# Performance work log

Measured on AMD Instinct MI355X. Metric: run time of the kernel, lower is better.

Reference implementation:

```python
import jax, jax.numpy as jnp
import numpy as np
import math

MODEL_DIM = 1024
B, S = 4, 2048


def setup_inputs() -> dict:
    key = jax.random.key(0)
    k_x, k_q, k_k, k_v = jax.random.split(key, 4)
    r5 = math.sqrt(5)
    x = jax.random.normal(k_x, (B, S, MODEL_DIM), dtype=jnp.float32)
    Q = jax.random.uniform(k_q, (MODEL_DIM, MODEL_DIM), minval=-r5, maxval=r5, dtype=jnp.float32)
    K = jax.random.uniform(k_k, (MODEL_DIM, MODEL_DIM), minval=-r5, maxval=r5, dtype=jnp.float32)
    V = jax.random.uniform(k_v, (MODEL_DIM, MODEL_DIM), minval=-r5, maxval=r5, dtype=jnp.float32)
    # attention_input == 'both' -> a == model_dim -> F is the full identity
    F = jnp.eye(MODEL_DIM, dtype=jnp.float32)
    return {"x": x, "Q": Q, "K": K, "V": V, "F": F}


def reference(x, Q, K, V, F):
    d = x.shape[-1]
    xf = jnp.matmul(x, F)
    Qx = jnp.matmul(xf, Q)          # [B,S,D]
    Kx = jnp.matmul(xf, K)          # [B,S,D]
    Vx = jnp.matmul(x, V)           # [B,S,D]
    scores = jnp.einsum('bqd,bkd->bqk', Qx, Kx) / math.sqrt(d)  # [B,S,S]
    seq = x.shape[1]
    mask = jnp.triu(jnp.ones((seq, seq), dtype=bool), k=1)
    scores = jnp.where(mask, -jnp.inf, scores)
    probs = jax.nn.softmax(scores, axis=-1)
    out = jnp.matmul(probs, Vx)     # [B,S,D]
    return (out, probs)
```

## Files before the change

kernel.cpp:

```cpp
#include <hip/hip_runtime.h>
#include <hip/hip_fp16.h>

typedef _Float16 f16;
typedef __attribute__((ext_vector_type(8))) _Float16 f16x8;
typedef __attribute__((ext_vector_type(4))) _Float16 f16x4;
typedef __attribute__((ext_vector_type(4))) float    f32x4;

#define D_MODEL 1024
#define SEQ     2048
#define BATCH   4
#define M_TOT   (BATCH * SEQ)
#define NE      ((long)M_TOT * D_MODEL)
#define WE      ((long)D_MODEL * D_MODEL)
#define OUT_ELEMS  ((long)M_TOT * D_MODEL)

static __device__ __forceinline__ f16x8 frag_read(const f16* lds, int row, int c)
{
    const f16x8* L = (const f16x8*)lds;
    return L[row * 4 + (c ^ ((row >> 1) & 3))];
}

static __device__ __forceinline__ void stage_tile(const f16* __restrict__ g, int row0,
                                                  int ld, int k0, f16* ldsbase,
                                                  int wave, int lane)
{
#pragma unroll
    for (int j = 0; j < 2; ++j) {
        const int chunk = wave * 2 + j;
        const int off16 = chunk * 64 + lane;
        const int row   = off16 >> 2;
        const int slot  = (off16 & 3) ^ ((row >> 1) & 3);
        const f16* src = g + (long)(row0 + row) * ld + (k0 + slot * 8);
        f16* dst = ldsbase + chunk * 512;
        __builtin_amdgcn_global_load_lds((const __attribute__((address_space(1))) void*)src,
                                         (__attribute__((address_space(3))) void*)dst,
                                         16, 0, 0);
    }
}

template<int ROWS>
static __device__ __forceinline__ void stage8(const f16* __restrict__ g, int row0,
                                              int ld, int k0, f16* dstbase,
                                              int wave, int lane)
{
#pragma unroll
    for (int j = 0; j < ROWS / 128; ++j) {
        const int off16 = j * 512 + wave * 64 + lane;
        const int row   = off16 >> 2;
        const int slot  = (off16 & 3) ^ ((row >> 1) & 3);
        const f16* src = g + (long)(row0 + row) * ld + (k0 + slot * 8);
        f16* dst = dstbase + (j * 512 + wave * 64) * 8;
        __builtin_amdgcn_global_load_lds((const __attribute__((address_space(1))) void*)src,
                                         (__attribute__((address_space(3))) void*)dst,
                                         16, 0, 0);
    }
}

#define BUFE 24576

template<int DUAL>
static __device__ __forceinline__ void g8_issueA(const f16* Ah, const f16* Al, int ld,
                                                 int m0, f16* lds, int t, int wave, int lane)
{
    f16* b = lds + (t & 1) * BUFE;
    stage8<256>(Ah, m0, ld, t * 32, b, wave, lane);
    if constexpr (DUAL) stage8<256>(Al, m0, ld, t * 32, b + 8192, wave, lane);
}
static __device__ __forceinline__ void g8_issueBh(const f16* BTh, int ld, int n0,
                                                  f16* lds, int t, int wave, int lane)
{
    stage8<128>(BTh, n0, ld, t * 32, lds + (t & 1) * BUFE + 16384, wave, lane);
}
static __device__ __forceinline__ void g8_issueBl(const f16* BTl, int ld, int n0,
                                                  f16* lds, int t, int wave, int lane)
{
    stage8<128>(BTl, n0, ld, t * 32, lds + (t & 1) * BUFE + 20480, wave, lane);
}

template<int DUAL>
static __device__ __forceinline__ void gemm8_pipe(
    const f16* __restrict__ Ah, const f16* __restrict__ Al,
    const f16* __restrict__ BTh, const f16* __restrict__ BTl,
    int ld, int m0, int n0, f16* lds, f32x4 acc[4][4], int wave, int lane)
{
    const int wr = wave >> 1, wc = wave & 1;
    const int cf = lane >> 4;

#pragma unroll
    for (int mi = 0; mi < 4; ++mi)
#pragma unroll
        for (int ni = 0; ni < 4; ++ni) acc[mi][ni] = (f32x4){0.f, 0.f, 0.f, 0.f};

    g8_issueA<DUAL>(Ah, Al, ld, m0, lds, 0, wave, lane);
    g8_issueBh(BTh, ld, n0, lds, 0, wave, lane);
    if constexpr (DUAL) g8_issueBl(BTl, ld, n0, lds, 0, wave, lane);
    g8_issueA<DUAL>(Ah, Al, ld, m0, lds, 1, wave, lane);
    g8_issueBh(BTh, ld, n0, lds, 1, wave, lane);

    for (int t = 0; t < 32; ++t) {
        if (t < 31) {
            if constexpr (DUAL) {
                g8_issueBl(BTl, ld, n0, lds, t + 1, wave, lane);
                asm volatile("s_waitcnt vmcnt(6)" ::: "memory");
            } else {
                asm volatile("s_waitcnt vmcnt(3)" ::: "memory");
            }
        } else {
            asm volatile("s_waitcnt vmcnt(0)" ::: "memory");
        }
        __builtin_amdgcn_sched_barrier(0);
        __builtin_amdgcn_s_barrier();
        __builtin_amdgcn_sched_barrier(0);

        f16* buf = lds + (t & 1) * BUFE;
        f16x8 fah[4], fal[4], fbh[4], fbl[4];
#pragma unroll
        for (int i = 0; i < 4; ++i) {
            const int ra = wr * 64 + i * 16 + (lane & 15);
            fah[i] = frag_read(buf, ra, cf);
            if constexpr (DUAL) fal[i] = frag_read(buf + 8192, ra, cf);
            const int rb = wc * 64 + i * 16 + (lane & 15);
            fbh[i] = frag_read(buf + 16384, rb, cf);
            if constexpr (DUAL) fbl[i] = frag_read(buf + 20480, rb, cf);
        }
        asm volatile("s_waitcnt lgkmcnt(0)" ::: "memory");
        __builtin_amdgcn_sched_barrier(0);
        __builtin_amdgcn_s_barrier();
        __builtin_amdgcn_sched_barrier(0);

        if (t < 30) {
            g8_issueA<DUAL>(Ah, Al, ld, m0, lds, t + 2, wave, lane);
            g8_issueBh(BTh, ld, n0, lds, t + 2, wave, lane);
        }
        __builtin_amdgcn_sched_barrier(0);

        __builtin_amdgcn_s_setprio(1);
#pragma unroll
        for (int mi = 0; mi < 4; ++mi)
#pragma unroll
            for (int ni = 0; ni < 4; ++ni)
                acc[mi][ni] = __builtin_amdgcn_mfma_f32_16x16x32_f16(fah[mi], fbh[ni], acc[mi][ni], 0, 0, 0);
        if constexpr (DUAL) {
#pragma unroll
            for (int mi = 0; mi < 4; ++mi)
#pragma unroll
                for (int ni = 0; ni < 4; ++ni)
                    acc[mi][ni] = __builtin_amdgcn_mfma_f32_16x16x32_f16(fah[mi], fbl[ni], acc[mi][ni], 0, 0, 0);
#pragma unroll
            for (int mi = 0; mi < 4; ++mi)
#pragma unroll
                for (int ni = 0; ni < 4; ++ni)
                    acc[mi][ni] = __builtin_amdgcn_mfma_f32_16x16x32_f16(fal[mi], fbh[ni], acc[mi][ni], 0, 0, 0);
        }
        __builtin_amdgcn_s_setprio(0);
    }
}

__global__ __launch_bounds__(512, 2) void k_gemm_T(
    const f16* __restrict__ xh, const f16* __restrict__ xl,
    const f16* __restrict__ WhT, const f16* __restrict__ WlT,
    f16* __restrict__ Th, f16* __restrict__ Tl)
{
    __shared__ __align__(16) f16 lds[49152];
    const int lane = threadIdx.x & 63, wave = threadIdx.x >> 6;
    const int L = blockIdx.x;
    const int swz = (L & 7) * 32 + (L >> 3);
    const int m0 = (swz >> 3) * 256;
    const int n0 = (swz & 7) * 128;
    f32x4 acc[4][4];
    gemm8_pipe<1>(xh, xl, WhT, WlT, D_MODEL, m0, n0, lds, acc, wave, lane);
    const int wr = wave >> 1, wc = wave & 1;
#pragma unroll
    for (int mi = 0; mi < 4; ++mi)
#pragma unroll
        for (int ni = 0; ni < 4; ++ni) {
            const int gn = n0 + wc * 64 + ni * 16 + (lane & 15);
#pragma unroll
            for (int r = 0; r < 4; ++r) {
                const int gm = m0 + wr * 64 + mi * 16 + (lane >> 4) * 4 + r;
                const float v = acc[mi][ni][r];
                const f16 h = (f16)v;
                Th[(long)gm * D_MODEL + gn] = h;
                Tl[(long)gm * D_MODEL + gn] = (f16)(v - (float)h);
            }
        }
}

__global__ __launch_bounds__(512, 2) void k_mega1(
    const f16* __restrict__ Th, const f16* __restrict__ Tl,
    const f16* __restrict__ xh, const f16* __restrict__ xl,
    const f16* __restrict__ VhT,
    float* __restrict__ scores, f16* __restrict__ VxT)
{
    __shared__ __align__(16) f16 lds[49152];
    const int lane = threadIdx.x & 63, wave = threadIdx.x >> 6;
    const int wr = wave >> 1, wc = wave & 1;
    f32x4 acc[4][4];

    if (blockIdx.x < 288) {
        const int L = blockIdx.x;
        const int swz = (L & 7) * 36 + (L >> 3);
        const int b = swz / 72;
        const int t = swz - b * 72;
        int qt = (int)((sqrtf(4.f * (float)t + 1.f) - 1.f) * 0.5f);
        while ((qt + 1) * (qt + 2) <= t) ++qt;
        while (qt * (qt + 1) > t) --qt;
        const int kt = t - qt * (qt + 1);

        const long ob = (long)b * SEQ * D_MODEL;
        gemm8_pipe<1>(Th + ob, Tl + ob, xh + ob, xl + ob, D_MODEL,
                      qt * 256, kt * 128, lds, acc, wave, lane);

        float* sb = scores + (long)b * SEQ * SEQ;
#pragma unroll
        for (int mi = 0; mi < 4; ++mi)
#pragma unroll
            for (int ni = 0; ni < 4; ++ni) {
                const int k = kt * 128 + wc * 64 + ni * 16 + (lane & 15);
#pragma unroll
                for (int r = 0; r < 4; ++r) {
                    const int q = qt * 256 + wr * 64 + mi * 16 + (lane >> 4) * 4 + r;
                    sb[(long)q * SEQ + k] = acc[mi][ni][r] * 0.03125f;
                }
            }
    } else {
        const int idx = blockIdx.x - 288;
        const int m0 = (idx >> 3) * 256;
        const int n0 = (idx & 7) * 128;
        gemm8_pipe<0>(xh, nullptr, VhT, nullptr, D_MODEL, m0, n0, lds, acc, wave, lane);
#pragma unroll
        for (int mi = 0; mi < 4; ++mi) {
            const int gm0 = m0 + wr * 64 + mi * 16 + (lane >> 4) * 4;
            const int b = gm0 >> 11, s = gm0 & 2047;
#pragma unroll
            for (int ni = 0; ni < 4; ++ni) {
                const int gn = n0 + wc * 64 + ni * 16 + (lane & 15);
                f16x4 p = {(f16)acc[mi][ni][0], (f16)acc[mi][ni][1],
                           (f16)acc[mi][ni][2], (f16)acc[mi][ni][3]};
                *(f16x4*)(VxT + ((long)b * D_MODEL + gn) * SEQ + s) = p;
            }
        }
    }
}

template<int DUAL>
static __device__ __forceinline__ void gemm_core(
    const f16* __restrict__ Ah, const f16* __restrict__ Al,
    const f16* __restrict__ BTh, const f16* __restrict__ BTl,
    int ld, int m0, int n0, int kEnd, f16* lds, f32x4 acc[4][4])
{
    const int t = threadIdx.x;
    const int lane = t & 63;
    const int wave = t >> 6;
    const int wr = wave >> 1, wc = wave & 1;
    const int cfrag = lane >> 4;

#pragma unroll
    for (int mi = 0; mi < 4; ++mi)
#pragma unroll
        for (int ni = 0; ni < 4; ++ni)
            acc[mi][ni] = (f32x4){0.f, 0.f, 0.f, 0.f};

    for (int k0 = 0; k0 < kEnd; k0 += 32) {
        stage_tile(Ah,  m0, ld, k0, lds,         wave, lane);
        stage_tile(BTh, n0, ld, k0, lds + 4096,  wave, lane);
        if (DUAL) {
            stage_tile(Al,  m0, ld, k0, lds + 8192,  wave, lane);
            stage_tile(BTl, n0, ld, k0, lds + 12288, wave, lane);
        }
        __syncthreads();

        f16x8 fah[4], fbh[4];
#pragma unroll
        for (int i = 0; i < 4; ++i) {
            fah[i] = frag_read(lds,        wr * 64 + i * 16 + (lane & 15), cfrag);
            fbh[i] = frag_read(lds + 4096, wc * 64 + i * 16 + (lane & 15), cfrag);
        }
        if (DUAL) {
            f16x8 fal[4], fbl[4];
#pragma unroll
            for (int i = 0; i < 4; ++i) {
                fal[i] = frag_read(lds + 8192,  wr * 64 + i * 16 + (lane & 15), cfrag);
                fbl[i] = frag_read(lds + 12288, wc * 64 + i * 16 + (lane & 15), cfrag);
            }
#pragma unroll
            for (int mi = 0; mi < 4; ++mi)
#pragma unroll
                for (int ni = 0; ni < 4; ++ni) {
                    acc[mi][ni] = __builtin_amdgcn_mfma_f32_16x16x32_f16(fah[mi], fbh[ni], acc[mi][ni], 0, 0, 0);
                    acc[mi][ni] = __builtin_amdgcn_mfma_f32_16x16x32_f16(fah[mi], fbl[ni], acc[mi][ni], 0, 0, 0);
                    acc[mi][ni] = __builtin_amdgcn_mfma_f32_16x16x32_f16(fal[mi], fbh[ni], acc[mi][ni], 0, 0, 0);
                }
        } else {
#pragma unroll
            for (int mi = 0; mi < 4; ++mi)
#pragma unroll
                for (int ni = 0; ni < 4; ++ni)
                    acc[mi][ni] = __builtin_amdgcn_mfma_f32_16x16x32_f16(fah[mi], fbh[ni], acc[mi][ni], 0, 0, 0);
        }
        __syncthreads();
    }
}

__global__ __launch_bounds__(256) void k_split_all(
    const float* __restrict__ x, const float* __restrict__ Q,
    const float* __restrict__ K, const float* __restrict__ V,
    f16* __restrict__ xh, f16* __restrict__ xl,
    f16* __restrict__ Qh, f16* __restrict__ Ql,
    f16* __restrict__ Kh, f16* __restrict__ Kl,
    f16* __restrict__ VhT)
{
    __shared__ float tile[32][33];
    const int bid = blockIdx.x;
    if (bid < 10240) {
        const float* src; f16 *dh, *dl; long off;
        if (bid < 8192)      { src = x; dh = xh; dl = xl; off = (long)bid * 1024; }
        else if (bid < 9216) { src = Q; dh = Qh; dl = Ql; off = (long)(bid - 8192) * 1024; }
        else                 { src = K; dh = Kh; dl = Kl; off = (long)(bid - 9216) * 1024; }
        const long i = off + threadIdx.x * 4;
        float4 v = *(const float4*)(src + i);
        f16 h0 = (f16)v.x, h1 = (f16)v.y, h2 = (f16)v.z, h3 = (f16)v.w;
        f16x4 hh = {h0, h1, h2, h3};
        f16x4 ll = {(f16)(v.x - (float)h0), (f16)(v.y - (float)h1),
                    (f16)(v.z - (float)h2), (f16)(v.w - (float)h3)};
        *(f16x4*)(dh + i) = hh;
        *(f16x4*)(dl + i) = ll;
    } else {
        const int idx = bid - 10240;
        const int n0 = (idx & 31) * 32, k0 = (idx >> 5) * 32;
        const int c = threadIdx.x & 31, r8 = threadIdx.x >> 5;
#pragma unroll
        for (int i = 0; i < 4; ++i) {
            const int r = r8 + i * 8;
            tile[r][c] = V[(long)(k0 + r) * D_MODEL + n0 + c];
        }
        __syncthreads();
#pragma unroll
        for (int i = 0; i < 4; ++i) {
            const int r = r8 + i * 8;
            VhT[(long)(n0 + r) * D_MODEL + k0 + c] = (f16)tile[c][r];
        }
    }
}

__global__ __launch_bounds__(256, 2) void k_gemm_w(
    const f16* __restrict__ Qh, const f16* __restrict__ Ql,
    const f16* __restrict__ Kh, const f16* __restrict__ Kl,
    f16* __restrict__ WhT, f16* __restrict__ WlT)
{
    __shared__ __align__(16) f16 lds[16384];
    f32x4 acc[4][4];
    const int m0 = blockIdx.y * 128, n0 = blockIdx.x * 128;
    gemm_core<1>(Qh, Ql, Kh, Kl, D_MODEL, m0, n0, D_MODEL, lds, acc);
    const int lane = threadIdx.x & 63, wave = threadIdx.x >> 6;
    const int wr = wave >> 1, wc = wave & 1;
#pragma unroll
    for (int mi = 0; mi < 4; ++mi)
#pragma unroll
        for (int ni = 0; ni < 4; ++ni) {
            const int gn = n0 + wc * 64 + ni * 16 + (lane & 15);
#pragma unroll
            for (int r = 0; r < 4; ++r) {
                const int gm = m0 + wr * 64 + mi * 16 + (lane >> 4) * 4 + r;
                const float v = acc[mi][ni][r];
                const f16 h = (f16)v;
                WhT[(long)gn * D_MODEL + gm] = h;
                WlT[(long)gn * D_MODEL + gm] = (f16)(v - (float)h);
            }
        }
}

__global__ __launch_bounds__(256) void k_softmax(float* __restrict__ probs,
                                                 f16* __restrict__ probs16)
{
    const long row = blockIdx.x;
    const int q = (int)(row & (SEQ - 1));
    float* s = probs + row * SEQ;
    const int t = threadIdx.x;
    const int kb = t * 8;
    float4 u0 = *(const float4*)(s + kb);
    float4 u1 = *(const float4*)(s + kb + 4);
    float v[8] = {u0.x, u0.y, u0.z, u0.w, u1.x, u1.y, u1.z, u1.w};
    float mx = -3.0e38f;
#pragma unroll
    for (int j = 0; j < 8; ++j) if (kb + j <= q) mx = fmaxf(mx, v[j]);
#pragma unroll
    for (int off = 32; off > 0; off >>= 1) mx = fmaxf(mx, __shfl_xor(mx, off, 64));
    __shared__ float redA[4], redB[4];
    const int lane = t & 63, wave = t >> 6;
    if (lane == 0) redA[wave] = mx;
    __syncthreads();
    mx = fmaxf(fmaxf(redA[0], redA[1]), fmaxf(redA[2], redA[3]));
    float e[8]; float sum = 0.f;
#pragma unroll
    for (int j = 0; j < 8; ++j) { e[j] = (kb + j <= q) ? __expf(v[j] - mx) : 0.f; sum += e[j]; }
#pragma unroll
    for (int off = 32; off > 0; off >>= 1) sum += __shfl_xor(sum, off, 64);
    if (lane == 0) redB[wave] = sum;
    __syncthreads();
    sum = (redB[0] + redB[1]) + (redB[2] + redB[3]);
    const float inv = 1.f / sum;
    float4 w0 = {e[0] * inv, e[1] * inv, e[2] * inv, e[3] * inv};
    float4 w1 = {e[4] * inv, e[5] * inv, e[6] * inv, e[7] * inv};
    *(float4*)(s + kb) = w0;
    *(float4*)(s + kb + 4) = w1;
    f16x8 p16 = {(f16)w0.x, (f16)w0.y, (f16)w0.z, (f16)w0.w,
                 (f16)w1.x, (f16)w1.y, (f16)w1.z, (f16)w1.w};
    *(f16x8*)(probs16 + row * SEQ + kb) = p16;
}

__global__ __launch_bounds__(256, 2) void k_gemm_pv(
    const f16* __restrict__ P, const f16* __restrict__ VT, float* __restrict__ out)
{
    const int dt = blockIdx.x, qt = 15 - blockIdx.y, b = blockIdx.z;
    __shared__ __align__(16) f16 lds[8192];
    f32x4 acc[4][4];
    const f16* Pb  = P  + (long)b * SEQ * SEQ;
    const f16* VTb = VT + (long)b * D_MODEL * SEQ;
    gemm_core<0>(Pb, nullptr, VTb, nullptr, SEQ, qt * 128, dt * 128, (qt + 1) * 128, lds, acc);
    float* ob = out + (long)b * SEQ * D_MODEL;
    const int lane = threadIdx.x & 63, wave = threadIdx.x >> 6;
    const int wr = wave >> 1, wc = wave & 1;
#pragma unroll
    for (int mi = 0; mi < 4; ++mi)
#pragma unroll
        for (int ni = 0; ni < 4; ++ni) {
            const int d = dt * 128 + wc * 64 + ni * 16 + (lane & 15);
#pragma unroll
            for (int r = 0; r < 4; ++r) {
                const int qq = qt * 128 + wr * 64 + mi * 16 + (lane >> 4) * 4 + r;
                ob[(long)qq * D_MODEL + d] = acc[mi][ni][r];
            }
        }
}

extern "C" void kernel_launch(void* const* d_in, const int* in_sizes, int n_in,
                              void* d_out, int out_size, void* d_ws, size_t ws_size,
                              hipStream_t stream)
{
    const float* x = (const float*)d_in[0];
    const float* Q = (const float*)d_in[1];
    const float* K = (const float*)d_in[2];
    const float* V = (const float*)d_in[3];

    float* out   = (float*)d_out;
    float* probs = out + OUT_ELEMS;

    f16* base = (f16*)d_ws;
    f16* xh   = base;
    f16* xl   = base + NE;
    f16* Th   = base + 2 * NE;
    f16* Tl   = base + 3 * NE;
    f16* VxT  = base + 4 * NE;
    f16* Qh   = base + 5 * NE;
    f16* Ql   = Qh + WE;
    f16* Kh   = Qh + 2 * WE;
    f16* Kl   = Qh + 3 * WE;
    f16* WhT  = Qh + 4 * WE;
    f16* WlT  = Qh + 5 * WE;
    f16* VhT  = Qh + 6 * WE;
    f16* probs16 = base + 2 * NE;

    k_split_all<<<11264, 256, 0, stream>>>(x, Q, K, V, xh, xl, Qh, Ql, Kh, Kl, VhT);
    k_gemm_w<<<dim3(8, 8), 256, 0, stream>>>(Qh, Ql, Kh, Kl, WhT, WlT);
    k_gemm_T<<<256, 512, 0, stream>>>(xh, xl, WhT, WlT, Th, Tl);
    k_mega1<<<544, 512, 0, stream>>>(Th, Tl, xh, xl, VhT, probs, VxT);
    k_softmax<<<8192, 256, 0, stream>>>(probs, probs16);
    k_gemm_pv<<<dim3(8, 16, 4), 256, 0, stream>>>(probs16, VxT, out);
}
```

Before: 274.3 us.

## Serialize dual-precision GEMM passes, shrink LDS, and move PV to pipelined 256x128 kernel

The dual-precision GEMM no longer loads hi and lo tiles together. It now runs three sequential K passes (hi*hi, hi*lo, lo*hi) through one half-size double-buffered pipeline. This cuts LDS per block so occupancy bounds rise from 2 to 4 blocks per CU. The PV product moves onto the same async global_load_lds pipeline with 256x128 tiles. The change also interleaves score and V blocks in the mega kernel, uses nontemporal stores for scores and probabilities, makes the split kernel handle 4 vectors per thread, and skips loading masked score entries in softmax. The risks are more pipeline iterations with fewer MFMAs each, and heavier register pressure at the higher occupancy target.

Measured after the change: 295.7 us. 7.8% more time.

```diff
diff --git a/kernel.cpp b/kernel.cpp
--- a/kernel.cpp
+++ b/kernel.cpp
@@ -56,32 +56,30 @@
     }
 }
 
-#define BUFE 24576
-
-template<int DUAL>
-static __device__ __forceinline__ void g8_issueA(const f16* Ah, const f16* Al, int ld,
-                                                 int m0, f16* lds, int t, int wave, int lane)
-{
-    f16* b = lds + (t & 1) * BUFE;
-    stage8<256>(Ah, m0, ld, t * 32, b, wave, lane);
-    if constexpr (DUAL) stage8<256>(Al, m0, ld, t * 32, b + 8192, wave, lane);
-}
-static __device__ __forceinline__ void g8_issueBh(const f16* BTh, int ld, int n0,
-                                                  f16* lds, int t, int wave, int lane)
-{
-    stage8<128>(BTh, n0, ld, t * 32, lds + (t & 1) * BUFE + 16384, wave, lane);
-}
-static __device__ __forceinline__ void g8_issueBl(const f16* BTl, int ld, int n0,
-                                                  f16* lds, int t, int wave, int lane)
-{
-    stage8<128>(BTl, n0, ld, t * 32, lds + (t & 1) * BUFE + 20480, wave, lane);
-}
-
-template<int DUAL>
-static __device__ __forceinline__ void gemm8_pipe(
-    const f16* __restrict__ Ah, const f16* __restrict__ Al,
-    const f16* __restrict__ BTh, const f16* __restrict__ BTl,
-    int ld, int m0, int n0, f16* lds, f32x4 acc[4][4], int wave, int lane)
+#define G8BUF 12288
+
+template<int TRIPLE>
+static __device__ __forceinline__ void g8_issue(const f16* A0, const f16* A1,
+    const f16* B0, const f16* B1, int ld, int m0, int n0, f16* lds, int t,
+    int wave, int lane)
+{
+    const f16* A; const f16* B; int k0;
+    if constexpr (TRIPLE) {
+        const int p = t >> 5;
+        A = (p == 2) ? A1 : A0;
+        B = (p == 1) ? B1 : B0;
+        k0 = (t & 31) << 5;
+    } else { A = A0; B = B0; k0 = t << 5; }
+    f16* b = lds + (t & 1) * G8BUF;
+    stage8<256>(A, m0, ld, k0, b, wave, lane);
+    stage8<128>(B, n0, ld, k0, b + 8192, wave, lane);
+}
+
+template<int TRIPLE>
+static __device__ __forceinline__ void gemm8s(
+    const f16* __restrict__ A0, const f16* __restrict__ A1,
+    const f16* __restrict__ B0, const f16* __restrict__ B1,
+    int ld, int m0, int n0, int nT, f16* lds, f32x4 acc[4][4], int wave, int lane)
 {
     const int wr = wave >> 1, wc = wave & 1;
     const int cf = lane >> 4;
@@ -91,20 +89,12 @@
 #pragma unroll
         for (int ni = 0; ni < 4; ++ni) acc[mi][ni] = (f32x4){0.f, 0.f, 0.f, 0.f};
 
-    g8_issueA<DUAL>(Ah, Al, ld, m0, lds, 0, wave, lane);
-    g8_issueBh(BTh, ld, n0, lds, 0, wave, lane);
-    if constexpr (DUAL) g8_issueBl(BTl, ld, n0, lds, 0, wave, lane);
-    g8_issueA<DUAL>(Ah, Al, ld, m0, lds, 1, wave, lane);
-    g8_issueBh(BTh, ld, n0, lds, 1, wave, lane);
-
-    for (int t = 0; t < 32; ++t) {
-        if (t < 31) {
-            if constexpr (DUAL) {
-                g8_issueBl(BTl, ld, n0, lds, t + 1, wave, lane);
-                asm volatile("s_waitcnt vmcnt(6)" ::: "memory");
-            } else {
-                asm volatile("s_waitcnt vmcnt(3)" ::: "memory");
-            }
+    g8_issue<TRIPLE>(A0, A1, B0, B1, ld, m0, n0, lds, 0, wave, lane);
+    g8_issue<TRIPLE>(A0, A1, B0, B1, ld, m0, n0, lds, 1, wave, lane);
+
+    for (int t = 0; t < nT; ++t) {
+        if (t < nT - 1) {
+            asm volatile("s_waitcnt vmcnt(3)" ::: "memory");
         } else {
             asm volatile("s_waitcnt vmcnt(0)" ::: "memory");
         }
@@ -112,26 +102,20 @@
         __builtin_amdgcn_s_barrier();
         __builtin_amdgcn_sched_barrier(0);
 
-        f16* buf = lds + (t & 1) * BUFE;
-        f16x8 fah[4], fal[4], fbh[4], fbl[4];
+        f16* buf = lds + (t & 1) * G8BUF;
+        f16x8 fa[4], fb[4];
 #pragma unroll
         for (int i = 0; i < 4; ++i) {
-            const int ra = wr * 64 + i * 16 + (lane & 15);
-            fah[i] = frag_read(buf, ra, cf);
-            if constexpr (DUAL) fal[i] = frag_read(buf + 8192, ra, cf);
-            const int rb = wc * 64 + i * 16 + (lane & 15);
-            fbh[i] = frag_read(buf + 16384, rb, cf);
-            if constexpr (DUAL) fbl[i] = frag_read(buf + 20480, rb, cf);
+            fa[i] = frag_read(buf,        wr * 64 + i * 16 + (lane & 15), cf);
+            fb[i] = frag_read(buf + 8192, wc * 64 + i * 16 + (lane & 15), cf);
         }
         asm volatile("s_waitcnt lgkmcnt(0)" ::: "memory");
         __builtin_amdgcn_sched_barrier(0);
         __builtin_amdgcn_s_barrier();
         __builtin_amdgcn_sched_barrier(0);
 
-        if (t < 30) {
-            g8_issueA<DUAL>(Ah, Al, ld, m0, lds, t + 2, wave, lane);
-            g8_issueBh(BTh, ld, n0, lds, t + 2, wave, lane);
-        }
+        if (t + 2 < nT)
+            g8_issue<TRIPLE>(A0, A1, B0, B1, ld, m0, n0, lds, t + 2, wave, lane);
         __builtin_amdgcn_sched_barrier(0);
 
         __builtin_amdgcn_s_setprio(1);
@@ -139,36 +123,24 @@
         for (int mi = 0; mi < 4; ++mi)
 #pragma unroll
             for (int ni = 0; ni < 4; ++ni)
-                acc[mi][ni] = __builtin_amdgcn_mfma_f32_16x16x32_f16(fah[mi], fbh[ni], acc[mi][ni], 0, 0, 0);
-        if constexpr (DUAL) {
-#pragma unroll
-            for (int mi = 0; mi < 4; ++mi)
-#pragma unroll
-                for (int ni = 0; ni < 4; ++ni)
-                    acc[mi][ni] = __builtin_amdgcn_mfma_f32_16x16x32_f16(fah[mi], fbl[ni], acc[mi][ni], 0, 0, 0);
-#pragma unroll
-            for (int mi = 0; mi < 4; ++mi)
-#pragma unroll
-                for (int ni = 0; ni < 4; ++ni)
-                    acc[mi][ni] = __builtin_amdgcn_mfma_f32_16x16x32_f16(fal[mi], fbh[ni], acc[mi][ni], 0, 0, 0);
-        }
+                acc[mi][ni] = __builtin_amdgcn_mfma_f32_16x16x32_f16(fa[mi], fb[ni], acc[mi][ni], 0, 0, 0);
         __builtin_amdgcn_s_setprio(0);
     }
 }
 
-__global__ __launch_bounds__(512, 2) void k_gemm_T(
+__global__ __launch_bounds__(512, 4) void k_gemm_T(
     const f16* __restrict__ xh, const f16* __restrict__ xl,
     const f16* __restrict__ WhT, const f16* __restrict__ WlT,
     f16* __restrict__ Th, f16* __restrict__ Tl)
 {
-    __shared__ __align__(16) f16 lds[49152];
+    __shared__ __align__(16) f16 lds[2 * G8BUF];
     const int lane = threadIdx.x & 63, wave = threadIdx.x >> 6;
     const int L = blockIdx.x;
     const int swz = (L & 7) * 32 + (L >> 3);
     const int m0 = (swz >> 3) * 256;
     const int n0 = (swz & 7) * 128;
     f32x4 acc[4][4];
-    gemm8_pipe<1>(xh, xl, WhT, WlT, D_MODEL, m0, n0, lds, acc, wave, lane);
+    gemm8s<1>(xh, xl, WhT, WlT, D_MODEL, m0, n0, 96, lds, acc, wave, lane);
     const int wr = wave >> 1, wc = wave & 1;
 #pragma unroll
     for (int mi = 0; mi < 4; ++mi)
@@ -186,30 +158,35 @@
         }
 }
 
-__global__ __launch_bounds__(512, 2) void k_mega1(
+__global__ __launch_bounds__(512, 4) void k_mega1(
     const f16* __restrict__ Th, const f16* __restrict__ Tl,
     const f16* __restrict__ xh, const f16* __restrict__ xl,
     const f16* __restrict__ VhT,
     float* __restrict__ scores, f16* __restrict__ VxT)
 {
-    __shared__ __align__(16) f16 lds[49152];
+    __shared__ __align__(16) f16 lds[2 * G8BUF];
     const int lane = threadIdx.x & 63, wave = threadIdx.x >> 6;
     const int wr = wave >> 1, wc = wave & 1;
+    const int bid = blockIdx.x;
+    int sidx = -1, vidx = -1;
+    if (bid < 512) {
+        const int g = bid >> 4, r = bid & 15;
+        if (r < 9) sidx = g * 9 + r;
+        else       vidx = g * 7 + (r - 9);
+    } else vidx = 224 + (bid - 512);
     f32x4 acc[4][4];
 
-    if (blockIdx.x < 288) {
-        const int L = blockIdx.x;
-        const int swz = (L & 7) * 36 + (L >> 3);
-        const int b = swz / 72;
-        const int t = swz - b * 72;
+    if (sidx >= 0) {
+        const int b = sidx / 72;
+        const int t = sidx - b * 72;
         int qt = (int)((sqrtf(4.f * (float)t + 1.f) - 1.f) * 0.5f);
         while ((qt + 1) * (qt + 2) <= t) ++qt;
         while (qt * (qt + 1) > t) --qt;
         const int kt = t - qt * (qt + 1);
 
         const long ob = (long)b * SEQ * D_MODEL;
-        gemm8_pipe<1>(Th + ob, Tl + ob, xh + ob, xl + ob, D_MODEL,
-                      qt * 256, kt * 128, lds, acc, wave, lane);
+        gemm8s<1>(Th + ob, Tl + ob, xh + ob, xl + ob, D_MODEL,
+                  qt * 256, kt * 128, 96, lds, acc, wave, lane);
 
         float* sb = scores + (long)b * SEQ * SEQ;
 #pragma unroll
@@ -220,14 +197,14 @@
 #pragma unroll
                 for (int r = 0; r < 4; ++r) {
                     const int q = qt * 256 + wr * 64 + mi * 16 + (lane >> 4) * 4 + r;
-                    sb[(long)q * SEQ + k] = acc[mi][ni][r] * 0.03125f;
+                    __builtin_nontemporal_store(acc[mi][ni][r] * 0.03125f,
+                                                &sb[(long)q * SEQ + k]);
                 }
             }
     } else {
-        const int idx = blockIdx.x - 288;
-        const int m0 = (idx >> 3) * 256;
-        const int n0 = (idx & 7) * 128;
-        gemm8_pipe<0>(xh, nullptr, VhT, nullptr, D_MODEL, m0, n0, lds, acc, wave, lane);
+        const int m0 = (vidx >> 3) * 256;
+        const int n0 = (vidx & 7) * 128;
+        gemm8s<0>(xh, nullptr, VhT, nullptr, D_MODEL, m0, n0, 32, lds, acc, wave, lane);
 #pragma unroll
         for (int mi = 0; mi < 4; ++mi) {
             const int gm0 = m0 + wr * 64 + mi * 16 + (lane >> 4) * 4;
@@ -243,8 +220,36 @@
     }
 }
 
-template<int DUAL>
-static __device__ __forceinline__ void gemm_core(
+__global__ __launch_bounds__(512, 4) void k_gemm_pv8(
+    const f16* __restrict__ P, const f16* __restrict__ VT, float* __restrict__ out)
+{
+    __shared__ __align__(16) f16 lds[2 * G8BUF];
+    const int lane = threadIdx.x & 63, wave = threadIdx.x >> 6;
+    const int i = blockIdx.x;
+    const int qt = 7 - (i >> 5);
+    const int dt = (i >> 2) & 7;
+    const int b  = i & 3;
+    const int nT = 8 * (qt + 1);
+    f32x4 acc[4][4];
+    const f16* Pb  = P  + (long)b * SEQ * SEQ;
+    const f16* VTb = VT + (long)b * D_MODEL * SEQ;
+    gemm8s<0>(Pb, nullptr, VTb, nullptr, SEQ, qt * 256, dt * 128, nT, lds, acc, wave, lane);
+    float* ob = out + (long)b * SEQ * D_MODEL;
+    const int wr = wave >> 1, wc = wave & 1;
+#pragma unroll
+    for (int mi = 0; mi < 4; ++mi)
+#pragma unroll
+        for (int ni = 0; ni < 4; ++ni) {
+            const int d = dt * 128 + wc * 64 + ni * 16 + (lane & 15);
+#pragma unroll
+            for (int r = 0; r < 4; ++r) {
+                const int qq = qt * 256 + wr * 64 + mi * 16 + (lane >> 4) * 4 + r;
+                ob[(long)qq * D_MODEL + d] = acc[mi][ni][r];
+            }
+        }
+}
+
+static __device__ __forceinline__ void gemm_core_dual(
     const f16* __restrict__ Ah, const f16* __restrict__ Al,
     const f16* __restrict__ BTh, const f16* __restrict__ BTl,
     int ld, int m0, int n0, int kEnd, f16* lds, f32x4 acc[4][4])
@@ -264,40 +269,26 @@
     for (int k0 = 0; k0 < kEnd; k0 += 32) {
         stage_tile(Ah,  m0, ld, k0, lds,         wave, lane);
         stage_tile(BTh, n0, ld, k0, lds + 4096,  wave, lane);
-        if (DUAL) {
-            stage_tile(Al,  m0, ld, k0, lds + 8192,  wave, lane);
-            stage_tile(BTl, n0, ld, k0, lds + 12288, wave, lane);
-        }
+        stage_tile(Al,  m0, ld, k0, lds + 8192,  wave, lane);
+        stage_tile(BTl, n0, ld, k0, lds + 12288, wave, lane);
         __syncthreads();
 
-        f16x8 fah[4], fbh[4];
+        f16x8 fah[4], fbh[4], fal[4], fbl[4];
 #pragma unroll
         for (int i = 0; i < 4; ++i) {
-            fah[i] = frag_read(lds,        wr * 64 + i * 16 + (lane & 15), cfrag);
-            fbh[i] = frag_read(lds + 4096, wc * 64 + i * 16 + (lane & 15), cfrag);
-        }
-        if (DUAL) {
-            f16x8 fal[4], fbl[4];
-#pragma unroll
-            for (int i = 0; i < 4; ++i) {
-                fal[i] = frag_read(lds + 8192,  wr * 64 + i * 16 + (lane & 15), cfrag);
-                fbl[i] = frag_read(lds + 12288, wc * 64 + i * 16 + (lane & 15), cfrag);
-            }
-#pragma unroll
-            for (int mi = 0; mi < 4; ++mi)
-#pragma unroll
-                for (int ni = 0; ni < 4; ++ni) {
-                    acc[mi][ni] = __builtin_amdgcn_mfma_f32_16x16x32_f16(fah[mi], fbh[ni], acc[mi][ni], 0, 0, 0);
-                    acc[mi][ni] = __builtin_amdgcn_mfma_f32_16x16x32_f16(fah[mi], fbl[ni], acc[mi][ni], 0, 0, 0);
-                    acc[mi][ni] = __builtin_amdgcn_mfma_f32_16x16x32_f16(fal[mi], fbh[ni], acc[mi][ni], 0, 0, 0);
-                }
-        } else {
-#pragma unroll
-            for (int mi = 0; mi < 4; ++mi)
-#pragma unroll
-                for (int ni = 0; ni < 4; ++ni)
-                    acc[mi][ni] = __builtin_amdgcn_mfma_f32_16x16x32_f16(fah[mi], fbh[ni], acc[mi][ni], 0, 0, 0);
-        }
+            fah[i] = frag_read(lds,         wr * 64 + i * 16 + (lane & 15), cfrag);
+            fbh[i] = frag_read(lds + 4096,  wc * 64 + i * 16 + (lane & 15), cfrag);
+            fal[i] = frag_read(lds + 8192,  wr * 64 + i * 16 + (lane & 15), cfrag);
+            fbl[i] = frag_read(lds + 12288, wc * 64 + i * 16 + (lane & 15), cfrag);
+        }
+#pragma unroll
+        for (int mi = 0; mi < 4; ++mi)
+#pragma unroll
+            for (int ni = 0; ni < 4; ++ni) {
+                acc[mi][ni] = __builtin_amdgcn_mfma_f32_16x16x32_f16(fah[mi], fbh[ni], acc[mi][ni], 0, 0, 0);
+                acc[mi][ni] = __builtin_amdgcn_mfma_f32_16x16x32_f16(fah[mi], fbl[ni], acc[mi][ni], 0, 0, 0);
+                acc[mi][ni] = __builtin_amdgcn_mfma_f32_16x16x32_f16(fal[mi], fbh[ni], acc[mi][ni], 0, 0, 0);
+            }
         __syncthreads();
     }
 }
@@ -312,21 +303,24 @@
 {
     __shared__ float tile[32][33];
     const int bid = blockIdx.x;
-    if (bid < 10240) {
-        const float* src; f16 *dh, *dl; long off;
-        if (bid < 8192)      { src = x; dh = xh; dl = xl; off = (long)bid * 1024; }
-        else if (bid < 9216) { src = Q; dh = Qh; dl = Ql; off = (long)(bid - 8192) * 1024; }
-        else                 { src = K; dh = Kh; dl = Kl; off = (long)(bid - 9216) * 1024; }
-        const long i = off + threadIdx.x * 4;
-        float4 v = *(const float4*)(src + i);
-        f16 h0 = (f16)v.x, h1 = (f16)v.y, h2 = (f16)v.z, h3 = (f16)v.w;
-        f16x4 hh = {h0, h1, h2, h3};
-        f16x4 ll = {(f16)(v.x - (float)h0), (f16)(v.y - (float)h1),
-                    (f16)(v.z - (float)h2), (f16)(v.w - (float)h3)};
-        *(f16x4*)(dh + i) = hh;
-        *(f16x4*)(dl + i) = ll;
+    if (bid < 2560) {
+        const float* src; f16 *dh, *dl; long base;
+        if (bid < 2048)      { src = x; dh = xh; dl = xl; base = (long)bid * 4096; }
+        else if (bid < 2304) { src = Q; dh = Qh; dl = Ql; base = (long)(bid - 2048) * 4096; }
+        else                 { src = K; dh = Kh; dl = Kl; base = (long)(bid - 2304) * 4096; }
+#pragma unroll
+        for (int j = 0; j < 4; ++j) {
+            const long i = base + (j * 256 + threadIdx.x) * 4;
+            float4 v = *(const float4*)(src + i);
+            f16 h0 = (f16)v.x, h1 = (f16)v.y, h2 = (f16)v.z, h3 = (f16)v.w;
+            f16x4 hh = {h0, h1, h2, h3};
+            f16x4 ll = {(f16)(v.x - (float)h0), (f16)(v.y - (float)h1),
+                        (f16)(v.z - (float)h2), (f16)(v.w - (float)h3)};
+            *(f16x4*)(dh + i) = hh;
+            *(f16x4*)(dl + i) = ll;
+        }
     } else {
-        const int idx = bid - 10240;
+        const int idx = bid - 2560;
         const int n0 = (idx & 31) * 32, k0 = (idx >> 5) * 32;
         const int c = threadIdx.x & 31, r8 = threadIdx.x >> 5;
 #pragma unroll
@@ -351,7 +345,7 @@
     __shared__ __align__(16) f16 lds[16384];
     f32x4 acc[4][4];
     const int m0 = blockIdx.y * 128, n0 = blockIdx.x * 128;
-    gemm_core<1>(Qh, Ql, Kh, Kl, D_MODEL, m0, n0, D_MODEL, lds, acc);
+    gemm_core_dual(Qh, Ql, Kh, Kl, D_MODEL, m0, n0, D_MODEL, lds, acc);
     const int lane = threadIdx.x & 63, wave = threadIdx.x >> 6;
     const int wr = wave >> 1, wc = wave & 1;
 #pragma unroll
@@ -378,9 +372,13 @@
     float* s = probs + row * SEQ;
     const int t = threadIdx.x;
     const int kb = t * 8;
-    float4 u0 = *(const float4*)(s + kb);
-    float4 u1 = *(const float4*)(s + kb + 4);
-    float v[8] = {u0.x, u0.y, u0.z, u0.w, u1.x, u1.y, u1.z, u1.w};
+    float v[8] = {0.f, 0.f, 0.f, 0.f, 0.f, 0.f, 0.f, 0.f};
+    if (kb <= q) {
+        float4 u0 = *(const float4*)(s + kb);
+        float4 u1 = *(const float4*)(s + kb + 4);
+        v[0] = u0.x; v[1] = u0.y; v[2] = u0.z; v[3] = u0.w;
+        v[4] = u1.x; v[5] = u1.y; v[6] = u1.z; v[7] = u1.w;
+    }
     float mx = -3.0e38f;
 #pragma unroll
     for (int j = 0; j < 8; ++j) if (kb + j <= q) mx = fmaxf(mx, v[j]);
@@ -400,38 +398,13 @@
     __syncthreads();
     sum = (redB[0] + redB[1]) + (redB[2] + redB[3]);
     const float inv = 1.f / sum;
-    float4 w0 = {e[0] * inv, e[1] * inv, e[2] * inv, e[3] * inv};
-    float4 w1 = {e[4] * inv, e[5] * inv, e[6] * inv, e[7] * inv};
-    *(float4*)(s + kb) = w0;
-    *(float4*)(s + kb + 4) = w1;
+    f32x4 w0 = {e[0] * inv, e[1] * inv, e[2] * inv, e[3] * inv};
+    f32x4 w1 = {e[4] * inv, e[5] * inv, e[6] * inv, e[7] * inv};
+    __builtin_nontemporal_store(w0, (f32x4*)(s + kb));
+    __builtin_nontemporal_store(w1, (f32x4*)(s + kb + 4));
     f16x8 p16 = {(f16)w0.x, (f16)w0.y, (f16)w0.z, (f16)w0.w,
                  (f16)w1.x, (f16)w1.y, (f16)w1.z, (f16)w1.w};
     *(f16x8*)(probs16 + row * SEQ + kb) = p16;
-}
-
-__global__ __launch_bounds__(256, 2) void k_gemm_pv(
-    const f16* __restrict__ P, const f16* __restrict__ VT, float* __restrict__ out)
-{
-    const int dt = blockIdx.x, qt = 15 - blockIdx.y, b = blockIdx.z;
-    __shared__ __align__(16) f16 lds[8192];
-    f32x4 acc[4][4];
-    const f16* Pb  = P  + (long)b * SEQ * SEQ;
-    const f16* VTb = VT + (long)b * D_MODEL * SEQ;
-    gemm_core<0>(Pb, nullptr, VTb, nullptr, SEQ, qt * 128, dt * 128, (qt + 1) * 128, lds, acc);
-    float* ob = out + (long)b * SEQ * D_MODEL;
-    const int lane = threadIdx.x & 63, wave = threadIdx.x >> 6;
-    const int wr = wave >> 1, wc = wave & 1;
-#pragma unroll
-    for (int mi = 0; mi < 4; ++mi)
-#pragma unroll
-        for (int ni = 0; ni < 4; ++ni) {
-            const int d = dt * 128 + wc * 64 + ni * 16 + (lane & 15);
-#pragma unroll
-            for (int r = 0; r < 4; ++r) {
-                const int qq = qt * 128 + wr * 64 + mi * 16 + (lane >> 4) * 4 + r;
-                ob[(long)qq * D_MODEL + d] = acc[mi][ni][r];
-            }
-        }
 }
 
 extern "C" void kernel_launch(void* const* d_in, const int* in_sizes, int n_in,
@@ -461,10 +434,10 @@
     f16* VhT  = Qh + 6 * WE;
     f16* probs16 = base + 2 * NE;
 
-    k_split_all<<<11264, 256, 0, stream>>>(x, Q, K, V, xh, xl, Qh, Ql, Kh, Kl, VhT);
+    k_split_all<<<3584, 256, 0, stream>>>(x, Q, K, V, xh, xl, Qh, Ql, Kh, Kl, VhT);
     k_gemm_w<<<dim3(8, 8), 256, 0, stream>>>(Qh, Ql, Kh, Kl, WhT, WlT);
     k_gemm_T<<<256, 512, 0, stream>>>(xh, xl, WhT, WlT, Th, Tl);
     k_mega1<<<544, 512, 0, stream>>>(Th, Tl, xh, xl, VhT, probs, VxT);
     k_softmax<<<8192, 256, 0, stream>>>(probs, probs16);
-    k_gemm_pv<<<dim3(8, 16, 4), 256, 0, stream>>>(probs16, VxT, out);
-}
+    k_gemm_pv8<<<256, 512, 0, stream>>>(probs16, VxT, out);
+}
```
